# Kernel optimization log

Hardware: AMD Instinct MI355X
Metric: run time of the kernel (lower is better)

Reference implementation:

```python
import jax, jax.numpy as jnp
import numpy as np

H = 256      # hidden_dim
ID = 512     # image_dim
TD = 512     # text_dim
NC = 80      # num_classes
NH = 4       # attention heads
HD = H // NH # head dim
B = 131072


def setup_inputs() -> dict:
    key = jax.random.key(0)
    ks = jax.random.split(key, 30)
    def rn(k, shape, scale=0.02):
        return jax.random.normal(k, shape, jnp.float32) * scale
    img = jax.random.normal(ks[0], (B, ID), jnp.float32)
    txt = jax.random.normal(ks[1], (B, TD), jnp.float32)
    r = jax.random.uniform(ks[2], (B,))
    img = img * (r >= 0.15).astype(jnp.float32)[:, None]
    txt = txt * (~((r >= 0.15) & (r < 0.30))).astype(jnp.float32)[:, None]
    return {
        'image_features': img,
        'text_features': txt,
        'W_ie': rn(ks[3], (ID, H)), 'b_ie': jnp.zeros((H,), jnp.float32),
        'W_te': rn(ks[4], (TD, H)), 'b_te': jnp.zeros((H,), jnp.float32),
        'fusion_query': rn(ks[5], (1, 1, H)),
        'Wq': rn(ks[6], (H, H)), 'bq': jnp.zeros((H,), jnp.float32),
        'Wk': rn(ks[7], (H, H)), 'bk': jnp.zeros((H,), jnp.float32),
        'Wv': rn(ks[8], (H, H)), 'bv': jnp.zeros((H,), jnp.float32),
        'Wo': rn(ks[9], (H, H)), 'bo': jnp.zeros((H,), jnp.float32),
        'W_ip': rn(ks[10], (H, 2 * H)), 'b_ip': jnp.zeros((2 * H,), jnp.float32),
        'W_tp': rn(ks[11], (H, 2 * H)), 'b_tp': jnp.zeros((2 * H,), jnp.float32),
        'W_fp': rn(ks[12], (H, 2 * H)), 'b_fp': jnp.zeros((2 * H,), jnp.float32),
        'Wc1': rn(ks[13], (2 * H, H)), 'bc1': jnp.zeros((H,), jnp.float32),
        'Wc2': rn(ks[14], (H, NC)), 'bc2': jnp.zeros((NC,), jnp.float32),
    }


def reference(image_features, text_features, W_ie, b_ie, W_te, b_te,
              fusion_query, Wq, bq, Wk, bk, Wv, bv, Wo, bo,
              W_ip, b_ip, W_tp, b_tp, W_fp, b_fp, Wc1, bc1, Wc2, bc2):
    # encoders (dropout inactive in eval)
    img_enc = jax.nn.relu(image_features @ W_ie + b_ie)   # [B,H]
    txt_enc = jax.nn.relu(text_features @ W_te + b_te)    # [B,H]

    img_present = jnp.linalg.norm(image_features, axis=1) > 1e-6
    txt_present = jnp.linalg.norm(text_features, axis=1) > 1e-6
    both = img_present & txt_present
    only_img = img_present & ~txt_present
    only_txt = ~img_present & txt_present

    # fusion branch: MHA pooling, query len 1, kv = two stacked modalities
    kv = jnp.stack([img_enc, txt_enc], axis=1)             # [B,2,H]
    q = (fusion_query.reshape(1, H) @ Wq + bq).reshape(NH, HD)      # [h,d]
    k = (kv @ Wk + bk).reshape(-1, 2, NH, HD)              # [B,2,h,d]
    v = (kv @ Wv + bv).reshape(-1, 2, NH, HD)
    scores = jnp.einsum('hd,bshd->bhs', q, k) / np.sqrt(HD)
    attn = jax.nn.softmax(scores, axis=-1)                 # [B,h,2]
    pooled = jnp.einsum('bhs,bshd->bhd', attn, v).reshape(-1, H)
    pooled = pooled @ Wo + bo                              # [B,H]
    fusion_out = pooled @ W_fp + b_fp                      # [B,2H]

    img_out = img_enc @ W_ip + b_ip                        # [B,2H]
    txt_out = txt_enc @ W_tp + b_tp                        # [B,2H]

    zero = jnp.zeros_like(fusion_out)
    fused = jnp.where(both[:, None], fusion_out,
            jnp.where(only_img[:, None], img_out,
            jnp.where(only_txt[:, None], txt_out, zero)))

    logits = jax.nn.relu(fused @ Wc1 + bc1) @ Wc2 + bc2    # [B,NC]
    return logits
```

## Files before the change

### kernel.cpp

```cpp
#include <hip/hip_runtime.h>
#include <hip/hip_fp16.h>
#include <math.h>

constexpr int H   = 256;
constexpr int ID  = 512;
constexpr int NC  = 80;
constexpr int BT  = 131072;

constexpr int MROWS = 48;
constexpr int NBLK  = (BT + MROWS - 1) / MROWS;

typedef _Float16 half8  __attribute__((ext_vector_type(8)));
typedef float    floatx4 __attribute__((ext_vector_type(4)));

#define MFMA16(a,b,c) __builtin_amdgcn_mfma_f32_16x16x32_f16((a),(b),(c),0,0,0)

__device__ inline half8 splat8(_Float16 v){ half8 r = {v,v,v,v,v,v,v,v}; return r; }

__device__ __align__(16) _Float16 g_WieT[H*ID];
__device__ __align__(16) _Float16 g_WteT[H*ID];
__device__ __align__(16) _Float16 g_WvT [H*H];
__device__ __align__(16) _Float16 g_WipT[2*H*H];
__device__ __align__(16) _Float16 g_WtpT[2*H*H];
__device__ __align__(16) _Float16 g_WofT[2*H*H];
__device__ __align__(16) _Float16 g_Wc1T[H*2*H];
__device__ __align__(16) _Float16 g_Wc2T[NC*H];
__device__ float g_wkeff[H*4];
__device__ float g_sbias[4];
__device__ float g_biasof[2*H];

constexpr int OFF_EI = 0;
constexpr int OFF_ET = 12672;
constexpr int OFF_PL = 25344;
constexpr int OFF_SUMI = 76032;
constexpr int OFF_SUMT = 76800;
constexpr int OFF_ATT  = 77568;
constexpr int OFF_SELB = 79104;
constexpr int OFF_SELI = 79296;
constexpr int OFF_SELT = 79488;
constexpr int SMEM_BYTES = 79680;

__global__ void aecf_setup(const float* __restrict__ W_ie, const float* __restrict__ W_te,
                           const float* __restrict__ fq,   const float* __restrict__ Wq,
                           const float* __restrict__ bq,   const float* __restrict__ Wk,
                           const float* __restrict__ bk,   const float* __restrict__ Wv,
                           const float* __restrict__ Wo,   const float* __restrict__ bo,
                           const float* __restrict__ W_ip, const float* __restrict__ W_tp,
                           const float* __restrict__ W_fp, const float* __restrict__ b_fp,
                           const float* __restrict__ Wc1,  const float* __restrict__ Wc2)
{
    __shared__ float qv[256];
    int b = blockIdx.x, t = threadIdx.x;

    if (b < 512) { int e = b*256+t; int k=e>>8, n=e&255; g_WieT[n*512+k] = (_Float16)W_ie[e]; return; }
    b -= 512;
    if (b < 512) { int e = b*256+t; int k=e>>8, n=e&255; g_WteT[n*512+k] = (_Float16)W_te[e]; return; }
    b -= 512;
    if (b < 256) { int e = b*256+t; int k=e>>8, n=e&255; g_WvT[n*256+k] = (_Float16)Wv[e]; return; }
    b -= 256;
    if (b < 512) { int e = b*256+t; int k=e>>9, n=e&511; g_WipT[n*256+k] = (_Float16)W_ip[e]; return; }
    b -= 512;
    if (b < 512) { int e = b*256+t; int k=e>>9, n=e&511; g_WtpT[n*256+k] = (_Float16)W_tp[e]; return; }
    b -= 512;
    if (b < 512) { int e = b*256+t; int k=e>>8, n=e&255; g_Wc1T[n*512+k] = (_Float16)Wc1[e]; return; }
    b -= 512;
    if (b < 80)  { int e = b*256+t; int k=e/80, n=e%80;  g_Wc2T[n*256+k] = (_Float16)Wc2[e]; return; }
    b -= 80;
    if (b < 512) {
        int n = b, c = t;
        float s = 0.f;
        for (int m = 0; m < 256; m++) s += Wo[c*256+m] * W_fp[m*512+n];
        g_WofT[n*256+c] = (_Float16)s;
        return;
    }
    b -= 512;
    if (b == 0) {
        float a = bq[t];
        for (int i = 0; i < 256; i++) a += fq[i] * Wq[i*256+t];
        qv[t] = a;
        __syncthreads();
        for (int h = 0; h < 4; h++) {
            float s = 0.f;
            for (int d = 0; d < 64; d++) s += Wk[t*256 + h*64+d] * qv[h*64+d];
            g_wkeff[t*4+h] = s * 0.125f;
        }
        if (t < 4) {
            float s = 0.f;
            for (int d = 0; d < 64; d++) s += bk[t*64+d] * qv[t*64+d];
            g_sbias[t] = s * 0.125f;
        }
        return;
    }
    b -= 1;
    {
        int n = b*256 + t;
        float s = b_fp[n];
        for (int m = 0; m < 256; m++) s += bo[m] * W_fp[m*512+n];
        g_biasof[n] = s;
    }
}

__global__ __launch_bounds__(256, 2)
void aecf_main(const float* __restrict__ img, const float* __restrict__ txt,
               const float* __restrict__ b_ie, const float* __restrict__ b_te,
               const float* __restrict__ bv,   const float* __restrict__ b_ip,
               const float* __restrict__ b_tp, const float* __restrict__ bc1,
               const float* __restrict__ bc2,  float* __restrict__ out)
{
    extern __shared__ char smem[];
    _Float16* encI  = (_Float16*)smem + OFF_EI;
    _Float16* encT  = (_Float16*)smem + OFF_ET;
    _Float16* pool  = (_Float16*)smem + OFF_PL;
    _Float16* fused = (_Float16*)smem;
    _Float16* h1    = pool;
    float* sumI = (float*)(smem + OFF_SUMI);
    float* sumT = (float*)(smem + OFF_SUMT);
    float* attn = (float*)(smem + OFF_ATT);
    float* selb = (float*)(smem + OFF_SELB);
    float* seli = (float*)(smem + OFF_SELI);
    float* selt = (float*)(smem + OFF_SELT);

    const int tid  = threadIdx.x;
    const int w    = tid >> 6;
    const int lane = tid & 63;
    const int l16  = lane & 15;
    const int q4   = lane >> 4;
    const int base = blockIdx.x * MROWS;

    auto encode = [&](const float* __restrict__ src, const _Float16* __restrict__ WT,
                      const float* __restrict__ bias, _Float16* dstE, float* sumLds) {
        floatx4 acc[3][4];
        #pragma unroll
        for (int rt = 0; rt < 3; rt++)
            #pragma unroll
            for (int ct = 0; ct < 4; ct++) acc[rt][ct] = (floatx4){0.f,0.f,0.f,0.f};
        float sab[3] = {0.f,0.f,0.f};
        int arow[3]; bool aok[3];
        #pragma unroll
        for (int rt = 0; rt < 3; rt++) { arow[rt] = base + rt*16 + l16; aok[rt] = arow[rt] < BT; }

        for (int ks = 0; ks < 16; ks++) {
            const int k0 = ks*32 + q4*8;
            half8 afr[3];
            #pragma unroll
            for (int rt = 0; rt < 3; rt++) {
                floatx4 x0 = {0.f,0.f,0.f,0.f}, x1 = {0.f,0.f,0.f,0.f};
                if (aok[rt]) {
                    const float* p = src + (size_t)arow[rt]*ID + k0;
                    x0 = *(const floatx4*)p;
                    x1 = *(const floatx4*)(p+4);
                }
                half8 a;
                a[0]=(_Float16)x0[0]; a[1]=(_Float16)x0[1]; a[2]=(_Float16)x0[2]; a[3]=(_Float16)x0[3];
                a[4]=(_Float16)x1[0]; a[5]=(_Float16)x1[1]; a[6]=(_Float16)x1[2]; a[7]=(_Float16)x1[3];
                afr[rt] = a;
                if (w == 0)
                    sab[rt] += fabsf(x0[0])+fabsf(x0[1])+fabsf(x0[2])+fabsf(x0[3])
                             + fabsf(x1[0])+fabsf(x1[1])+fabsf(x1[2])+fabsf(x1[3]);
            }
            #pragma unroll
            for (int ct = 0; ct < 4; ct++) {
                const int ng = w*64 + ct*16 + l16;
                half8 bfr = *(const half8*)(WT + (size_t)ng*512 + k0);
                #pragma unroll
                for (int rt = 0; rt < 3; rt++) acc[rt][ct] = MFMA16(afr[rt], bfr, acc[rt][ct]);
            }
        }
        #pragma unroll
        for (int ct = 0; ct < 4; ct++) {
            const int colg = w*64 + ct*16 + l16;
            const float bb = bias[colg];
            #pragma unroll
            for (int rt = 0; rt < 3; rt++)
                #pragma unroll
                for (int r = 0; r < 4; r++) {
                    float v = acc[rt][ct][r] + bb;
                    v = v > 0.f ? v : 0.f;
                    dstE[(rt*16 + q4*4 + r)*264 + colg] = (_Float16)v;
                }
        }
        if (w == 0) {
            #pragma unroll
            for (int rt = 0; rt < 3; rt++) sumLds[(rt*16 + l16)*4 + q4] = sab[rt];
        }
    };
    encode(img, g_WieT, b_ie, encI, sumI);
    encode(txt, g_WteT, b_te, encT, sumT);
    __syncthreads();

    if (tid < 192) {
        const int row = tid >> 2, h = tid & 3;
        float sI = sumI[row*4]+sumI[row*4+1]+sumI[row*4+2]+sumI[row*4+3];
        float sT = sumT[row*4]+sumT[row*4+1]+sumT[row*4+2]+sumT[row*4+3];
        bool pi = sI > 0.f, pt = sT > 0.f;
        if (h == 0) {
            selb[row] = (pi && pt)  ? 1.f : 0.f;
            seli[row] = (pi && !pt) ? 1.f : 0.f;
            selt[row] = (!pi && pt) ? 1.f : 0.f;
        }
        float s0 = g_sbias[h], s1 = s0;
        for (int c = 0; c < H; c++) {
            const float wk = g_wkeff[c*4+h];
            s0 += wk * (float)encI[row*264+c];
            s1 += wk * (float)encT[row*264+c];
        }
        const float a0 = 1.f / (1.f + __expf(s1 - s0));
        attn[(row*4+h)*2]   = a0;
        attn[(row*4+h)*2+1] = 1.f - a0;
    }
    __syncthreads();

    floatx4 pacc[3][8];
    #pragma unroll
    for (int rt = 0; rt < 3; rt++)
        #pragma unroll
        for (int ct = 0; ct < 8; ct++) pacc[rt][ct] = (floatx4){0.f,0.f,0.f,0.f};

    {
        _Float16 s[3];
        #pragma unroll
        for (int rt = 0; rt < 3; rt++) s[rt] = (_Float16)seli[rt*16 + l16];
        for (int ks = 0; ks < 8; ks++) {
            const int k0 = ks*32 + q4*8;
            half8 afr[3];
            #pragma unroll
            for (int rt = 0; rt < 3; rt++)
                afr[rt] = (*(const half8*)(encI + (rt*16+l16)*264 + k0)) * splat8(s[rt]);
            #pragma unroll
            for (int ct = 0; ct < 8; ct++) {
                const int ng = w*128 + ct*16 + l16;
                half8 bfr = *(const half8*)(g_WipT + (size_t)ng*256 + k0);
                #pragma unroll
                for (int rt = 0; rt < 3; rt++) pacc[rt][ct] = MFMA16(afr[rt], bfr, pacc[rt][ct]);
            }
        }
    }
    {
        _Float16 s[3];
        #pragma unroll
        for (int rt = 0; rt < 3; rt++) s[rt] = (_Float16)selt[rt*16 + l16];
        for (int ks = 0; ks < 8; ks++) {
            const int k0 = ks*32 + q4*8;
            half8 afr[3];
            #pragma unroll
            for (int rt = 0; rt < 3; rt++)
                afr[rt] = (*(const half8*)(encT + (rt*16+l16)*264 + k0)) * splat8(s[rt]);
            #pragma unroll
            for (int ct = 0; ct < 8; ct++) {
                const int ng = w*128 + ct*16 + l16;
                half8 bfr = *(const half8*)(g_WtpT + (size_t)ng*256 + k0);
                #pragma unroll
                for (int rt = 0; rt < 3; rt++) pacc[rt][ct] = MFMA16(afr[rt], bfr, pacc[rt][ct]);
            }
        }
    }

    floatx4 poolacc[4][3];
    #pragma unroll
    for (int h = 0; h < 4; h++)
        #pragma unroll
        for (int rt = 0; rt < 3; rt++) poolacc[h][rt] = (floatx4){0.f,0.f,0.f,0.f};

    #pragma unroll
    for (int h = 0; h < 4; h++) {
        _Float16 a0l[3], a1l[3];
        #pragma unroll
        for (int rt = 0; rt < 3; rt++) {
            const int rr = rt*16 + l16;
            a0l[rt] = (_Float16)attn[(rr*4+h)*2];
            a1l[rt] = (_Float16)attn[(rr*4+h)*2+1];
        }
        const int ng = h*64 + w*16 + l16;
        for (int ks = 0; ks < 8; ks++) {
            const int k0 = ks*32 + q4*8;
            half8 bfr = *(const half8*)(g_WvT + (size_t)ng*256 + k0);
            #pragma unroll
            for (int rt = 0; rt < 3; rt++) {
                half8 eI = *(const half8*)(encI + (rt*16+l16)*264 + k0);
                half8 eT = *(const half8*)(encT + (rt*16+l16)*264 + k0);
                half8 m  = eI * splat8(a0l[rt]) + eT * splat8(a1l[rt]);
                poolacc[h][rt] = MFMA16(m, bfr, poolacc[h][rt]);
            }
        }
    }
    __syncthreads();

    #pragma unroll
    for (int h = 0; h < 4; h++) {
        const int colg = h*64 + w*16 + l16;
        const float bvv = bv[colg];
        #pragma unroll
        for (int rt = 0; rt < 3; rt++)
            #pragma unroll
            for (int r = 0; r < 4; r++) {
                const int row = rt*16 + q4*4 + r;
                pool[row*264 + colg] = (_Float16)((poolacc[h][rt][r] + bvv) * selb[row]);
            }
    }
    __syncthreads();

    for (int ks = 0; ks < 8; ks++) {
        const int k0 = ks*32 + q4*8;
        half8 afr[3];
        #pragma unroll
        for (int rt = 0; rt < 3; rt++)
            afr[rt] = *(const half8*)(pool + (rt*16+l16)*264 + k0);
        #pragma unroll
        for (int ct = 0; ct < 8; ct++) {
            const int ng = w*128 + ct*16 + l16;
            half8 bfr = *(const half8*)(g_WofT + (size_t)ng*256 + k0);
            #pragma unroll
            for (int rt = 0; rt < 3; rt++) pacc[rt][ct] = MFMA16(afr[rt], bfr, pacc[rt][ct]);
        }
    }

    {
        float sB[12], sI2[12], sT2[12];
        #pragma unroll
        for (int rt = 0; rt < 3; rt++)
            #pragma unroll
            for (int r = 0; r < 4; r++) {
                const int row = rt*16 + q4*4 + r;
                sB[rt*4+r] = selb[row]; sI2[rt*4+r] = seli[row]; sT2[rt*4+r] = selt[row];
            }
        #pragma unroll
        for (int ct = 0; ct < 8; ct++) {
            const int colg = w*128 + ct*16 + l16;
            const float bof = g_biasof[colg], bip = b_ip[colg], btp = b_tp[colg];
            #pragma unroll
            for (int rt = 0; rt < 3; rt++)
                #pragma unroll
                for (int r = 0; r < 4; r++) {
                    const int row = rt*16 + q4*4 + r;
                    const float f = pacc[rt][ct][r] + sB[rt*4+r]*bof + sI2[rt*4+r]*bip + sT2[rt*4+r]*btp;
                    fused[row*520 + colg] = (_Float16)f;
                }
        }
    }
    __syncthreads();

    floatx4 cacc[3][4];
    #pragma unroll
    for (int rt = 0; rt < 3; rt++)
        #pragma unroll
        for (int ct = 0; ct < 4; ct++) cacc[rt][ct] = (floatx4){0.f,0.f,0.f,0.f};
    for (int ks = 0; ks < 16; ks++) {
        const int k0 = ks*32 + q4*8;
        half8 afr[3];
        #pragma unroll
        for (int rt = 0; rt < 3; rt++)
            afr[rt] = *(const half8*)(fused + (rt*16+l16)*520 + k0);
        #pragma unroll
        for (int ct = 0; ct < 4; ct++) {
            const int ng = w*64 + ct*16 + l16;
            half8 bfr = *(const half8*)(g_Wc1T + (size_t)ng*512 + k0);
            #pragma unroll
            for (int rt = 0; rt < 3; rt++) cacc[rt][ct] = MFMA16(afr[rt], bfr, cacc[rt][ct]);
        }
    }
    #pragma unroll
    for (int ct = 0; ct < 4; ct++) {
        const int colg = w*64 + ct*16 + l16;
        const float b1 = bc1[colg];
        #pragma unroll
        for (int rt = 0; rt < 3; rt++)
            #pragma unroll
            for (int r = 0; r < 4; r++) {
                float v = cacc[rt][ct][r] + b1;
                v = v > 0.f ? v : 0.f;
                h1[(rt*16 + q4*4 + r)*264 + colg] = (_Float16)v;
            }
    }
    __syncthreads();

    for (int p = w; p < 15; p += 4) {
        const int rt = p / 5, ct = p % 5;
        const int ng = ct*16 + l16;
        floatx4 a2 = (floatx4){0.f,0.f,0.f,0.f};
        for (int ks = 0; ks < 8; ks++) {
            const int k0 = ks*32 + q4*8;
            half8 afr = *(const half8*)(h1 + (rt*16+l16)*264 + k0);
            half8 bfr = *(const half8*)(g_Wc2T + (size_t)ng*256 + k0);
            a2 = MFMA16(afr, bfr, a2);
        }
        const float b2 = bc2[ng];
        #pragma unroll
        for (int r = 0; r < 4; r++) {
            const int rowg = base + rt*16 + q4*4 + r;
            if (rowg < BT) out[(size_t)rowg*NC + ng] = a2[r] + b2;
        }
    }
}

extern "C" void kernel_launch(void* const* d_in, const int* in_sizes, int n_in,
                              void* d_out, int out_size, void* d_ws, size_t ws_size,
                              hipStream_t stream)
{
    const float* img  = (const float*)d_in[0];
    const float* txt  = (const float*)d_in[1];
    const float* W_ie = (const float*)d_in[2];
    const float* b_ie = (const float*)d_in[3];
    const float* W_te = (const float*)d_in[4];
    const float* b_te = (const float*)d_in[5];
    const float* fq   = (const float*)d_in[6];
    const float* Wq   = (const float*)d_in[7];
    const float* bq   = (const float*)d_in[8];
    const float* Wk   = (const float*)d_in[9];
    const float* bk   = (const float*)d_in[10];
    const float* Wv   = (const float*)d_in[11];
    const float* bv   = (const float*)d_in[12];
    const float* Wo   = (const float*)d_in[13];
    const float* bo   = (const float*)d_in[14];
    const float* W_ip = (const float*)d_in[15];
    const float* b_ip = (const float*)d_in[16];
    const float* W_tp = (const float*)d_in[17];
    const float* b_tp = (const float*)d_in[18];
    const float* W_fp = (const float*)d_in[19];
    const float* b_fp = (const float*)d_in[20];
    const float* Wc1  = (const float*)d_in[21];
    const float* bc1  = (const float*)d_in[22];
    const float* Wc2  = (const float*)d_in[23];
    const float* bc2  = (const float*)d_in[24];
    float* out = (float*)d_out;

    hipFuncSetAttribute((const void*)aecf_main,
                        hipFuncAttributeMaxDynamicSharedMemorySize, SMEM_BYTES);

    aecf_setup<<<3411, 256, 0, stream>>>(W_ie, W_te, fq, Wq, bq, Wk, bk, Wv,
                                         Wo, bo, W_ip, W_tp, W_fp, b_fp, Wc1, Wc2);
    aecf_main<<<NBLK, 256, SMEM_BYTES, stream>>>(img, txt, b_ie, b_te, bv,
                                                 b_ip, b_tp, bc1, bc2, out);
}
```

Before: 1.706 ms.

## Shrink row tile to 32 and raise occupancy to three blocks per CU

Cuts the per-block row tile from 48 to 32 rows, shrinking LDS use and accumulator registers so launch bounds can target three blocks per CU. The attention-pooling projection is moved ahead of the image/text projections and its result written to LDS before them, which lowers peak live accumulators. The score dot products now use vectorised LDS loads with a head-major wkeff layout, and bounds checks are dropped because the batch divides the tile evenly. The trade-off is less weight reuse per block, since each weight fragment now feeds two MFMA row tiles instead of three, plus an extra barrier.

```diff
diff --git a/kernel.cpp b/kernel.cpp
--- a/kernel.cpp
+++ b/kernel.cpp
@@ -7,8 +7,8 @@
 constexpr int NC  = 80;
 constexpr int BT  = 131072;
 
-constexpr int MROWS = 48;
-constexpr int NBLK  = (BT + MROWS - 1) / MROWS;
+constexpr int MROWS = 32;
+constexpr int NBLK  = BT / MROWS;
 
 typedef _Float16 half8  __attribute__((ext_vector_type(8)));
 typedef float    floatx4 __attribute__((ext_vector_type(4)));
@@ -25,20 +25,20 @@
 __device__ __align__(16) _Float16 g_WofT[2*H*H];
 __device__ __align__(16) _Float16 g_Wc1T[H*2*H];
 __device__ __align__(16) _Float16 g_Wc2T[NC*H];
-__device__ float g_wkeff[H*4];
+__device__ __align__(16) float g_wkeff[4*H];
 __device__ float g_sbias[4];
 __device__ float g_biasof[2*H];
 
 constexpr int OFF_EI = 0;
-constexpr int OFF_ET = 12672;
-constexpr int OFF_PL = 25344;
-constexpr int OFF_SUMI = 76032;
-constexpr int OFF_SUMT = 76800;
-constexpr int OFF_ATT  = 77568;
-constexpr int OFF_SELB = 79104;
-constexpr int OFF_SELI = 79296;
-constexpr int OFF_SELT = 79488;
-constexpr int SMEM_BYTES = 79680;
+constexpr int OFF_ET = 8448;
+constexpr int OFF_PL = 16896;
+constexpr int OFF_SUMI = 50688;
+constexpr int OFF_SUMT = 51200;
+constexpr int OFF_ATT  = 51712;
+constexpr int OFF_SELB = 52736;
+constexpr int OFF_SELI = 52864;
+constexpr int OFF_SELT = 52992;
+constexpr int SMEM_BYTES = 53120;
 
 __global__ void aecf_setup(const float* __restrict__ W_ie, const float* __restrict__ W_te,
                            const float* __restrict__ fq,   const float* __restrict__ Wq,
@@ -82,7 +82,7 @@
         for (int h = 0; h < 4; h++) {
             float s = 0.f;
             for (int d = 0; d < 64; d++) s += Wk[t*256 + h*64+d] * qv[h*64+d];
-            g_wkeff[t*4+h] = s * 0.125f;
+            g_wkeff[h*256 + t] = s * 0.125f;
         }
         if (t < 4) {
             float s = 0.f;
@@ -100,7 +100,7 @@
     }
 }
 
-__global__ __launch_bounds__(256, 2)
+__global__ __launch_bounds__(256, 3)
 void aecf_main(const float* __restrict__ img, const float* __restrict__ txt,
                const float* __restrict__ b_ie, const float* __restrict__ b_te,
                const float* __restrict__ bv,   const float* __restrict__ b_ip,
@@ -129,27 +129,21 @@
 
     auto encode = [&](const float* __restrict__ src, const _Float16* __restrict__ WT,
                       const float* __restrict__ bias, _Float16* dstE, float* sumLds) {
-        floatx4 acc[3][4];
-        #pragma unroll
-        for (int rt = 0; rt < 3; rt++)
+        floatx4 acc[2][4];
+        #pragma unroll
+        for (int rt = 0; rt < 2; rt++)
             #pragma unroll
             for (int ct = 0; ct < 4; ct++) acc[rt][ct] = (floatx4){0.f,0.f,0.f,0.f};
-        float sab[3] = {0.f,0.f,0.f};
-        int arow[3]; bool aok[3];
-        #pragma unroll
-        for (int rt = 0; rt < 3; rt++) { arow[rt] = base + rt*16 + l16; aok[rt] = arow[rt] < BT; }
+        float sab[2] = {0.f, 0.f};
 
         for (int ks = 0; ks < 16; ks++) {
             const int k0 = ks*32 + q4*8;
-            half8 afr[3];
-            #pragma unroll
-            for (int rt = 0; rt < 3; rt++) {
-                floatx4 x0 = {0.f,0.f,0.f,0.f}, x1 = {0.f,0.f,0.f,0.f};
-                if (aok[rt]) {
-                    const float* p = src + (size_t)arow[rt]*ID + k0;
-                    x0 = *(const floatx4*)p;
-                    x1 = *(const floatx4*)(p+4);
-                }
+            half8 afr[2];
+            #pragma unroll
+            for (int rt = 0; rt < 2; rt++) {
+                const float* p = src + (size_t)(base + rt*16 + l16)*ID + k0;
+                floatx4 x0 = *(const floatx4*)p;
+                floatx4 x1 = *(const floatx4*)(p+4);
                 half8 a;
                 a[0]=(_Float16)x0[0]; a[1]=(_Float16)x0[1]; a[2]=(_Float16)x0[2]; a[3]=(_Float16)x0[3];
                 a[4]=(_Float16)x1[0]; a[5]=(_Float16)x1[1]; a[6]=(_Float16)x1[2]; a[7]=(_Float16)x1[3];
@@ -163,7 +157,7 @@
                 const int ng = w*64 + ct*16 + l16;
                 half8 bfr = *(const half8*)(WT + (size_t)ng*512 + k0);
                 #pragma unroll
-                for (int rt = 0; rt < 3; rt++) acc[rt][ct] = MFMA16(afr[rt], bfr, acc[rt][ct]);
+                for (int rt = 0; rt < 2; rt++) acc[rt][ct] = MFMA16(afr[rt], bfr, acc[rt][ct]);
             }
         }
         #pragma unroll
@@ -171,7 +165,7 @@
             const int colg = w*64 + ct*16 + l16;
             const float bb = bias[colg];
             #pragma unroll
-            for (int rt = 0; rt < 3; rt++)
+            for (int rt = 0; rt < 2; rt++)
                 #pragma unroll
                 for (int r = 0; r < 4; r++) {
                     float v = acc[rt][ct][r] + bb;
@@ -181,14 +175,14 @@
         }
         if (w == 0) {
             #pragma unroll
-            for (int rt = 0; rt < 3; rt++) sumLds[(rt*16 + l16)*4 + q4] = sab[rt];
+            for (int rt = 0; rt < 2; rt++) sumLds[(rt*16 + l16)*4 + q4] = sab[rt];
         }
     };
     encode(img, g_WieT, b_ie, encI, sumI);
     encode(txt, g_WteT, b_te, encT, sumT);
     __syncthreads();
 
-    if (tid < 192) {
+    if (tid < 128) {
         const int row = tid >> 2, h = tid & 3;
         float sI = sumI[row*4]+sumI[row*4+1]+sumI[row*4+2]+sumI[row*4+3];
         float sT = sumT[row*4]+sumT[row*4+1]+sumT[row*4+2]+sumT[row*4+3];
@@ -199,10 +193,18 @@
             selt[row] = (!pi && pt) ? 1.f : 0.f;
         }
         float s0 = g_sbias[h], s1 = s0;
-        for (int c = 0; c < H; c++) {
-            const float wk = g_wkeff[c*4+h];
-            s0 += wk * (float)encI[row*264+c];
-            s1 += wk * (float)encT[row*264+c];
+        const _Float16* rI = encI + row*264;
+        const _Float16* rT = encT + row*264;
+        const float* wkh = g_wkeff + h*256;
+        for (int c8 = 0; c8 < 256; c8 += 8) {
+            half8 eI = *(const half8*)(rI + c8);
+            half8 eT = *(const half8*)(rT + c8);
+            floatx4 wa = *(const floatx4*)(wkh + c8);
+            floatx4 wb = *(const floatx4*)(wkh + c8 + 4);
+            s0 += wa[0]*(float)eI[0] + wa[1]*(float)eI[1] + wa[2]*(float)eI[2] + wa[3]*(float)eI[3]
+                + wb[0]*(float)eI[4] + wb[1]*(float)eI[5] + wb[2]*(float)eI[6] + wb[3]*(float)eI[7];
+            s1 += wa[0]*(float)eT[0] + wa[1]*(float)eT[1] + wa[2]*(float)eT[2] + wa[3]*(float)eT[3]
+                + wb[0]*(float)eT[4] + wb[1]*(float)eT[5] + wb[2]*(float)eT[6] + wb[3]*(float)eT[7];
         }
         const float a0 = 1.f / (1.f + __expf(s1 - s0));
         attn[(row*4+h)*2]   = a0;
@@ -210,114 +212,116 @@
     }
     __syncthreads();
 
-    floatx4 pacc[3][8];
+    {
+        floatx4 poolacc[4][2];
+        #pragma unroll
+        for (int h = 0; h < 4; h++)
+            #pragma unroll
+            for (int rt = 0; rt < 2; rt++) poolacc[h][rt] = (floatx4){0.f,0.f,0.f,0.f};
+
+        #pragma unroll
+        for (int h = 0; h < 4; h++) {
+            _Float16 a0l[2], a1l[2];
+            #pragma unroll
+            for (int rt = 0; rt < 2; rt++) {
+                const int rr = rt*16 + l16;
+                a0l[rt] = (_Float16)attn[(rr*4+h)*2];
+                a1l[rt] = (_Float16)attn[(rr*4+h)*2+1];
+            }
+            const int ng = h*64 + w*16 + l16;
+            for (int ks = 0; ks < 8; ks++) {
+                const int k0 = ks*32 + q4*8;
+                half8 bfr = *(const half8*)(g_WvT + (size_t)ng*256 + k0);
+                #pragma unroll
+                for (int rt = 0; rt < 2; rt++) {
+                    half8 eI = *(const half8*)(encI + (rt*16+l16)*264 + k0);
+                    half8 eT = *(const half8*)(encT + (rt*16+l16)*264 + k0);
+                    half8 m  = eI * splat8(a0l[rt]) + eT * splat8(a1l[rt]);
+                    poolacc[h][rt] = MFMA16(m, bfr, poolacc[h][rt]);
+                }
+            }
+        }
+        #pragma unroll
+        for (int h = 0; h < 4; h++) {
+            const int colg = h*64 + w*16 + l16;
+            const float bvv = bv[colg];
+            #pragma unroll
+            for (int rt = 0; rt < 2; rt++)
+                #pragma unroll
+                for (int r = 0; r < 4; r++) {
+                    const int row = rt*16 + q4*4 + r;
+                    pool[row*264 + colg] = (_Float16)((poolacc[h][rt][r] + bvv) * selb[row]);
+                }
+        }
+    }
+    __syncthreads();
+
+    floatx4 pacc[2][8];
     #pragma unroll
-    for (int rt = 0; rt < 3; rt++)
+    for (int rt = 0; rt < 2; rt++)
         #pragma unroll
         for (int ct = 0; ct < 8; ct++) pacc[rt][ct] = (floatx4){0.f,0.f,0.f,0.f};
 
     {
-        _Float16 s[3];
-        #pragma unroll
-        for (int rt = 0; rt < 3; rt++) s[rt] = (_Float16)seli[rt*16 + l16];
+        _Float16 s[2];
+        #pragma unroll
+        for (int rt = 0; rt < 2; rt++) s[rt] = (_Float16)seli[rt*16 + l16];
         for (int ks = 0; ks < 8; ks++) {
             const int k0 = ks*32 + q4*8;
-            half8 afr[3];
-            #pragma unroll
-            for (int rt = 0; rt < 3; rt++)
+            half8 afr[2];
+            #pragma unroll
+            for (int rt = 0; rt < 2; rt++)
                 afr[rt] = (*(const half8*)(encI + (rt*16+l16)*264 + k0)) * splat8(s[rt]);
             #pragma unroll
             for (int ct = 0; ct < 8; ct++) {
                 const int ng = w*128 + ct*16 + l16;
                 half8 bfr = *(const half8*)(g_WipT + (size_t)ng*256 + k0);
                 #pragma unroll
-                for (int rt = 0; rt < 3; rt++) pacc[rt][ct] = MFMA16(afr[rt], bfr, pacc[rt][ct]);
-            }
-        }
-    }
-    {
-        _Float16 s[3];
-        #pragma unroll
-        for (int rt = 0; rt < 3; rt++) s[rt] = (_Float16)selt[rt*16 + l16];
+                for (int rt = 0; rt < 2; rt++) pacc[rt][ct] = MFMA16(afr[rt], bfr, pacc[rt][ct]);
+            }
+        }
+    }
+    {
+        _Float16 s[2];
+        #pragma unroll
+        for (int rt = 0; rt < 2; rt++) s[rt] = (_Float16)selt[rt*16 + l16];
         for (int ks = 0; ks < 8; ks++) {
             const int k0 = ks*32 + q4*8;
-            half8 afr[3];
-            #pragma unroll
-            for (int rt = 0; rt < 3; rt++)
+            half8 afr[2];
+            #pragma unroll
+            for (int rt = 0; rt < 2; rt++)
                 afr[rt] = (*(const half8*)(encT + (rt*16+l16)*264 + k0)) * splat8(s[rt]);
             #pragma unroll
             for (int ct = 0; ct < 8; ct++) {
                 const int ng = w*128 + ct*16 + l16;
                 half8 bfr = *(const half8*)(g_WtpT + (size_t)ng*256 + k0);
                 #pragma unroll
-                for (int rt = 0; rt < 3; rt++) pacc[rt][ct] = MFMA16(afr[rt], bfr, pacc[rt][ct]);
-            }
-        }
-    }
-
-    floatx4 poolacc[4][3];
-    #pragma unroll
-    for (int h = 0; h < 4; h++)
-        #pragma unroll
-        for (int rt = 0; rt < 3; rt++) poolacc[h][rt] = (floatx4){0.f,0.f,0.f,0.f};
-
-    #pragma unroll
-    for (int h = 0; h < 4; h++) {
-        _Float16 a0l[3], a1l[3];
-        #pragma unroll
-        for (int rt = 0; rt < 3; rt++) {
-            const int rr = rt*16 + l16;
-            a0l[rt] = (_Float16)attn[(rr*4+h)*2];
-            a1l[rt] = (_Float16)attn[(rr*4+h)*2+1];
-        }
-        const int ng = h*64 + w*16 + l16;
+                for (int rt = 0; rt < 2; rt++) pacc[rt][ct] = MFMA16(afr[rt], bfr, pacc[rt][ct]);
+            }
+        }
+    }
+    {
         for (int ks = 0; ks < 8; ks++) {
             const int k0 = ks*32 + q4*8;
-            half8 bfr = *(const half8*)(g_WvT + (size_t)ng*256 + k0);
-            #pragma unroll
-            for (int rt = 0; rt < 3; rt++) {
-                half8 eI = *(const half8*)(encI + (rt*16+l16)*264 + k0);
-                half8 eT = *(const half8*)(encT + (rt*16+l16)*264 + k0);
-                half8 m  = eI * splat8(a0l[rt]) + eT * splat8(a1l[rt]);
-                poolacc[h][rt] = MFMA16(m, bfr, poolacc[h][rt]);
-            }
-        }
-    }
-    __syncthreads();
-
-    #pragma unroll
-    for (int h = 0; h < 4; h++) {
-        const int colg = h*64 + w*16 + l16;
-        const float bvv = bv[colg];
-        #pragma unroll
-        for (int rt = 0; rt < 3; rt++)
-            #pragma unroll
-            for (int r = 0; r < 4; r++) {
-                const int row = rt*16 + q4*4 + r;
-                pool[row*264 + colg] = (_Float16)((poolacc[h][rt][r] + bvv) * selb[row]);
-            }
-    }
-    __syncthreads();
-
-    for (int ks = 0; ks < 8; ks++) {
-        const int k0 = ks*32 + q4*8;
-        half8 afr[3];
-        #pragma unroll
-        for (int rt = 0; rt < 3; rt++)
-            afr[rt] = *(const half8*)(pool + (rt*16+l16)*264 + k0);
-        #pragma unroll
-        for (int ct = 0; ct < 8; ct++) {
-            const int ng = w*128 + ct*16 + l16;
-            half8 bfr = *(const half8*)(g_WofT + (size_t)ng*256 + k0);
-            #pragma unroll
-            for (int rt = 0; rt < 3; rt++) pacc[rt][ct] = MFMA16(afr[rt], bfr, pacc[rt][ct]);
-        }
-    }
-
-    {
-        float sB[12], sI2[12], sT2[12];
-        #pragma unroll
-        for (int rt = 0; rt < 3; rt++)
+            half8 afr[2];
+            #pragma unroll
+            for (int rt = 0; rt < 2; rt++)
+                afr[rt] = *(const half8*)(pool + (rt*16+l16)*264 + k0);
+            #pragma unroll
+            for (int ct = 0; ct < 8; ct++) {
+                const int ng = w*128 + ct*16 + l16;
+                half8 bfr = *(const half8*)(g_WofT + (size_t)ng*256 + k0);
+                #pragma unroll
+                for (int rt = 0; rt < 2; rt++) pacc[rt][ct] = MFMA16(afr[rt], bfr, pacc[rt][ct]);
+            }
+        }
+    }
+    __syncthreads();
+
+    {
+        float sB[8], sI2[8], sT2[8];
+        #pragma unroll
+        for (int rt = 0; rt < 2; rt++)
             #pragma unroll
             for (int r = 0; r < 4; r++) {
                 const int row = rt*16 + q4*4 + r;
@@ -328,7 +332,7 @@
             const int colg = w*128 + ct*16 + l16;
             const float bof = g_biasof[colg], bip = b_ip[colg], btp = b_tp[colg];
             #pragma unroll
-            for (int rt = 0; rt < 3; rt++)
+            for (int rt = 0; rt < 2; rt++)
                 #pragma unroll
                 for (int r = 0; r < 4; r++) {
                     const int row = rt*16 + q4*4 + r;
@@ -339,41 +343,44 @@
     }
     __syncthreads();
 
-    floatx4 cacc[3][4];
-    #pragma unroll
-    for (int rt = 0; rt < 3; rt++)
-        #pragma unroll
-        for (int ct = 0; ct < 4; ct++) cacc[rt][ct] = (floatx4){0.f,0.f,0.f,0.f};
-    for (int ks = 0; ks < 16; ks++) {
-        const int k0 = ks*32 + q4*8;
-        half8 afr[3];
-        #pragma unroll
-        for (int rt = 0; rt < 3; rt++)
-            afr[rt] = *(const half8*)(fused + (rt*16+l16)*520 + k0);
+    {
+        floatx4 cacc[2][4];
+        #pragma unroll
+        for (int rt = 0; rt < 2; rt++)
+            #pragma unroll
+            for (int ct = 0; ct < 4; ct++) cacc[rt][ct] = (floatx4){0.f,0.f,0.f,0.f};
+        for (int ks = 0; ks < 16; ks++) {
+            const int k0 = ks*32 + q4*8;
+            half8 afr[2];
+            #pragma unroll
+            for (int rt = 0; rt < 2; rt++)
+                afr[rt] = *(const half8*)(fused + (rt*16+l16)*520 + k0);
+            #pragma unroll
+            for (int ct = 0; ct < 4; ct++) {
+                const int ng = w*64 + ct*16 + l16;
+                half8 bfr = *(const half8*)(g_Wc1T + (size_t)ng*512 + k0);
+                #pragma unroll
+                for (int rt = 0; rt < 2; rt++) cacc[rt][ct] = MFMA16(afr[rt], bfr, cacc[rt][ct]);
+            }
+        }
+        __syncthreads();
         #pragma unroll
         for (int ct = 0; ct < 4; ct++) {
-            const int ng = w*64 + ct*16 + l16;
-            half8 bfr = *(const half8*)(g_Wc1T + (size_t)ng*512 + k0);
-            #pragma unroll
-            for (int rt = 0; rt < 3; rt++) cacc[rt][ct] = MFMA16(afr[rt], bfr, cacc[rt][ct]);
-        }
-    }
-    #pragma unroll
-    for (int ct = 0; ct < 4; ct++) {
-        const int colg = w*64 + ct*16 + l16;
-        const float b1 = bc1[colg];
-        #pragma unroll
-        for (int rt = 0; rt < 3; rt++)
-            #pragma unroll
-            for (int r = 0; r < 4; r++) {
-                float v = cacc[rt][ct][r] + b1;
-                v = v > 0.f ? v : 0.f;
-                h1[(rt*16 + q4*4 + r)*264 + colg] = (_Float16)v;
-            }
-    }
-    __syncthreads();
-
-    for (int p = w; p < 15; p += 4) {
+            const int colg = w*64 + ct*16 + l16;
+            const float b1 = bc1[colg];
+            #pragma unroll
+            for (int rt = 0; rt < 2; rt++)
+                #pragma unroll
+                for (int r = 0; r < 4; r++) {
+                    float v = cacc[rt][ct][r] + b1;
+                    v = v > 0.f ? v : 0.f;
+                    h1[(rt*16 + q4*4 + r)*264 + colg] = (_Float16)v;
+                }
+        }
+    }
+    __syncthreads();
+
+    for (int p = w; p < 10; p += 4) {
         const int rt = p / 5, ct = p % 5;
         const int ng = ct*16 + l16;
         floatx4 a2 = (floatx4){0.f,0.f,0.f,0.f};
@@ -387,7 +394,7 @@
         #pragma unroll
         for (int r = 0; r < 4; r++) {
             const int rowg = base + rt*16 + q4*4 + r;
-            if (rowg < BT) out[(size_t)rowg*NC + ng] = a2[r] + b2;
+            out[(size_t)rowg*NC + ng] = a2[r] + b2;
         }
     }
 }
```

After: 1.661 ms. -2.6%, faster.
